# Kernel optimization log

Measured on AMD Instinct MI355X. Metric: run time of the kernel, lower is better.

The kernel has to match this reference:

```python
import jax, jax.numpy as jnp
import numpy as np

R0 = 1.0
DIM_A, DIM_V, DIM_D = 32, 32, 32
N_NODES = 20000
N_EDGES = 640000


def radial_encode_8(r, r0):
    # 8 Gaussian radial basis functions on the edge length |r_ij|
    d = jnp.linalg.norm(r, axis=-1)                      # [E]
    centers = jnp.linspace(0.0, r0, 8)                   # [8]
    width = r0 / 8.0
    return jnp.exp(-(((d[..., None] - centers) / width) ** 2))  # [E,8]


def tens_sigmoid_vec(v):
    # norm-saturating nonlinearity for rank-1 tensors (direction-preserving)
    n2 = jnp.sum(v * v, axis=-1, keepdims=True)
    return v * jax.lax.rsqrt(1.0 + n2)


def setup_inputs() -> dict:
    key = jax.random.key(0)
    ks = jax.random.split(key, 12)

    def lin(k, fan_in, fan_out):
        return jax.random.normal(k, (fan_in, fan_out), jnp.float32) / np.float32(np.sqrt(fan_in))

    return dict(
        r_ij=jax.random.normal(ks[0], (N_EDGES, 3), jnp.float32),
        w_rad=lin(ks[1], 8, DIM_A), b_rad=jnp.zeros((DIM_A,), jnp.float32),
        w_direct=lin(ks[2], DIM_A, DIM_A),
        w1=lin(ks[3], DIM_A, 2 * DIM_A), b1=jnp.zeros((2 * DIM_A,), jnp.float32),
        w2=lin(ks[4], 2 * DIM_A, 2 * DIM_A), b2=jnp.zeros((2 * DIM_A,), jnp.float32),
        w3=lin(ks[5], 2 * DIM_A, DIM_A), b3=jnp.zeros((DIM_A,), jnp.float32),
        w_v=lin(ks[6], DIM_A, DIM_V),
        w_d=lin(ks[7], DIM_A, DIM_D),
        edges_src=jax.random.randint(ks[8], (N_EDGES,), 0, N_NODES),
        n_nodes=N_NODES,
    )


def reference(r_ij, w_rad, b_rad, w_direct, w1, b1, w2, b2, w3, b3, w_v, w_d,
              edges_src, n_nodes):
    lrelu = lambda x: jnp.where(x > 0, x, 0.1 * x)
    # radial MLP: Linear(8, a) -> MLP (lin_direct + 3-layer leakyrelu net)
    h = radial_encode_8(r_ij, R0) @ w_rad + b_rad                      # [E,a]
    rad = h @ w_direct + (lrelu(lrelu(h @ w1 + b1) @ w2 + b2) @ w3 + b3)  # [E,a]
    rs = tens_sigmoid_vec(r_ij * (7.0 / R0))                            # [E,3]

    seg = lambda x: jax.ops.segment_sum(x, edges_src, num_segments=n_nodes)
    A_a = seg(rad)                                                      # [N,a]
    A_v = seg(rad[:, :, None] * rs[:, None, :])                         # [N,a,3]
    # phi_d_ij = rad ⊗ rs ⊗ rs per edge  -> [E,a,3,3], then scatter-sum
    A_d = seg(rad[:, :, None, None] * rs[:, None, None, :] * rs[:, None, :, None])  # [N,a,3,3]

    out_v = jnp.einsum('nac,av->nvc', A_v, w_v)                         # TensLinear rank 1
    out_d = jnp.einsum('naij,ad->ndij', A_d, w_d)                       # TensLinear rank 2
    return A_a, out_v, out_d
```

## Files before the change

### kernel.cpp

```cpp
#include <hip/hip_runtime.h>
#include <hip/hip_bf16.h>
#include <hip/hip_fp16.h>
#include <math.h>


#define TSIZE 8192
#define DMAX  2.0f
#define EPB   4
#define HB    128
#define TILE  10240
#define NPB   4

#define O_WRAD 0
#define O_BRAD 256
#define O_WDIR 288
#define O_W1   1312
#define O_B1   3360
#define O_W2   3424
#define O_B2   7520
#define O_W3   7584
#define O_B3   9632
#define O_WV   9664
#define O_WD   10688
#define W_TOT  11712

__device__ __forceinline__ float lrelu(float x) { return x > 0.0f ? x : 0.1f * x; }

__device__ __forceinline__ float ldf(const void* p, int i, bool f32) {
    return f32 ? ((const float*)p)[i]
               : __uint_as_float(((unsigned int)((const unsigned short*)p)[i]) << 16);
}
__device__ __forceinline__ void stf(void* p, size_t i, float v, bool f32) {
    if (f32) ((float*)p)[i] = v;
    else     ((__hip_bfloat16*)p)[i] = __float2bfloat16(v);
}

__device__ __forceinline__ bool detect_f32(const void* r) {
    const unsigned short* p = (const unsigned short*)r;
    int bad = 0;
#pragma unroll 8
    for (int i = 0; i < 128; i++) {
        float v = __uint_as_float(((unsigned int)p[i]) << 16);
        bad |= (!isfinite(v) || fabsf(v) > 1e5f) ? 1 : 0;
    }
    return bad != 0;
}

__global__ void k_prep(const void* __restrict__ r_ij,
                       const void* w_rad, const void* b_rad, const void* w_direct,
                       const void* w1, const void* b1, const void* w2, const void* b2,
                       const void* w3, const void* b3, const void* w_v, const void* w_d,
                       float* __restrict__ wcat, int* __restrict__ flag,
                       int* __restrict__ counts, int N) {
    const int b = blockIdx.x;
    if (b == 0) {
        if (threadIdx.x == 0) flag[0] = detect_f32(r_ij) ? 1 : 0;
    } else if (b <= 11) {
        const bool f32 = detect_f32(r_ij);
        const void* src; int cnt; int off;
        switch (b) {
            case 1:  src = w_rad;    cnt = 256;  off = O_WRAD; break;
            case 2:  src = b_rad;    cnt = 32;   off = O_BRAD; break;
            case 3:  src = w_direct; cnt = 1024; off = O_WDIR; break;
            case 4:  src = w1;       cnt = 2048; off = O_W1;   break;
            case 5:  src = b1;       cnt = 64;   off = O_B1;   break;
            case 6:  src = w2;       cnt = 4096; off = O_W2;   break;
            case 7:  src = b2;       cnt = 64;   off = O_B2;   break;
            case 8:  src = w3;       cnt = 2048; off = O_W3;   break;
            case 9:  src = b3;       cnt = 32;   off = O_B3;   break;
            case 10: src = w_v;      cnt = 1024; off = O_WV;   break;
            default: src = w_d;      cnt = 1024; off = O_WD;   break;
        }
        for (int i = threadIdx.x; i < cnt; i += blockDim.x)
            wcat[off + i] = ldf(src, i, f32);
    } else if (counts) {
        int i = (b - 12) * blockDim.x + threadIdx.x;
        if (i < N) counts[i] = 0;
    }
}

__global__ void __launch_bounds__(64 * EPB) k_table(const float* __restrict__ wcat,
                                                    float* __restrict__ tabI) {
    __shared__ float Lh[EPB][32], Lt1[EPB][64], Lt2[EPB][64], Lrad[EPB][32];

    const int s = threadIdx.x >> 6;
    const int j = threadIdx.x & 63;
    const int e = blockIdx.x * EPB + s;
    const float d = (float)e * (DMAX / (float)(TSIZE - 1));

    float enc[8];
#pragma unroll
    for (int k = 0; k < 8; k++) {
        float t = (d - (float)k * (1.0f / 7.0f)) * 8.0f;
        enc[k] = expf(-t * t);
    }

    if (j < 32) {
        float hv = wcat[O_BRAD + j];
#pragma unroll
        for (int k = 0; k < 8; k++) hv = fmaf(enc[k], wcat[O_WRAD + k * 32 + j], hv);
        Lh[s][j] = hv;
    }
    __syncthreads();

    {
        float v = wcat[O_B1 + j];
#pragma unroll
        for (int i = 0; i < 32; i++) v = fmaf(Lh[s][i], wcat[O_W1 + i * 64 + j], v);
        Lt1[s][j] = lrelu(v);
    }
    __syncthreads();

    {
        float v = wcat[O_B2 + j];
#pragma unroll
        for (int i = 0; i < 64; i++) v = fmaf(Lt1[s][i], wcat[O_W2 + i * 64 + j], v);
        Lt2[s][j] = lrelu(v);
    }
    __syncthreads();

    if (j < 32) {
        float v = wcat[O_B3 + j];
#pragma unroll
        for (int i = 0; i < 64; i++) v = fmaf(Lt2[s][i], wcat[O_W3 + i * 32 + j], v);
#pragma unroll
        for (int i = 0; i < 32; i++) v = fmaf(Lh[s][i], wcat[O_WDIR + i * 32 + j], v);
        Lrad[s][j] = v;
        tabI[e * 96 + j] = v;
    }
    __syncthreads();

    if (j < 32) {
        float sv = 0.0f, sd = 0.0f;
#pragma unroll
        for (int i = 0; i < 32; i++) {
            float ri = Lrad[s][i];
            sv = fmaf(ri, wcat[O_WV + i * 32 + j], sv);
            sd = fmaf(ri, wcat[O_WD + i * 32 + j], sd);
        }
        tabI[e * 96 + 32 + j] = sv;
        tabI[e * 96 + 64 + j] = sd;
    }
}

__global__ void __launch_bounds__(256) k_hist(const int* __restrict__ src, int E,
                                              int chunk,
                                              unsigned short* __restrict__ cnt,
                                              int N) {
    __shared__ int lcnt[TILE];
    const int b = blockIdx.x % HB;
    const int t = blockIdx.x / HB;
    const int lo = b * chunk;
    const int hi = min(lo + chunk, E);
    const int t0 = t * TILE;
    const int tl = min(TILE, N - t0);

    for (int i = threadIdx.x; i < tl; i += 256) lcnt[i] = 0;
    __syncthreads();
    for (int e = lo + threadIdx.x; e < hi; e += 256) {
        const int s = src[e] - t0;
        if ((unsigned)s < (unsigned)tl) atomicAdd(&lcnt[s], 1);
    }
    __syncthreads();
    unsigned short* out = cnt + (size_t)(t * HB + b) * TILE;
    for (int i = threadIdx.x; i < tl; i += 256)
        out[i] = (unsigned short)lcnt[i];
}

__global__ void __launch_bounds__(64) k_colscan(unsigned short* __restrict__ cnt,
                                                int* __restrict__ tot,
                                                int* __restrict__ coarse, int N) {
    const int lane = threadIdx.x;
    const int n = blockIdx.x * 64 + lane;
    int run = 0;
    if (n < N) {
        const int t = n / TILE;
        const int nl = n % TILE;
        unsigned short* col = cnt + (size_t)(t * HB) * TILE + nl;
#pragma unroll 4
        for (int b = 0; b < HB; b++) {
            int c = col[(size_t)b * TILE];
            col[(size_t)b * TILE] = (unsigned short)run;
            run += c;
        }
        tot[n] = run;
    }
    int s = run;
    for (int off = 32; off > 0; off >>= 1) s += __shfl_down(s, off);
    if (lane == 0) coarse[blockIdx.x] = s;
}

__global__ void __launch_bounds__(64) k_scan2(const int* __restrict__ tot,
                                              const int* __restrict__ coarse,
                                              int* __restrict__ rowstart, int N) {
    const int lane = threadIdx.x;
    const int b = blockIdx.x;
    int cp = 0;
    for (int j = lane; j < b; j += 64) cp += coarse[j];
    for (int off = 32; off > 0; off >>= 1) cp += __shfl_down(cp, off);
    const int cpre = __shfl(cp, 0);

    const int n = b * 64 + lane;
    const int v = (n < N) ? tot[n] : 0;
    int inc = v;
    for (int off = 1; off < 64; off <<= 1) {
        int y = __shfl_up(inc, off);
        if (lane >= off) inc += y;
    }
    if (n < N) rowstart[n] = cpre + inc - v;
    if (n == N - 1) rowstart[N] = cpre + inc;
}

template <bool P16>
__global__ void __launch_bounds__(256) k_place(
        const int* __restrict__ src, int E, int chunk,
        const unsigned short* __restrict__ cnt, const int* __restrict__ rowstart,
        const void* __restrict__ r_ij, const int* __restrict__ flag,
        void* __restrict__ epsv, int N) {
    __shared__ int cur[TILE];
    const int b = blockIdx.x % HB;
    const int t = blockIdx.x / HB;
    const int lo = b * chunk;
    const int hi = min(lo + chunk, E);
    const int t0 = t * TILE;
    const int tl = min(TILE, N - t0);
    const bool f32 = flag[0] != 0;

    const unsigned short* base = cnt + (size_t)(t * HB + b) * TILE;
    for (int i = threadIdx.x; i < tl; i += 256)
        cur[i] = rowstart[t0 + i] + (int)base[i];
    __syncthreads();
    for (int e = lo + threadIdx.x; e < hi; e += 256) {
        const int s = src[e] - t0;
        if ((unsigned)s < (unsigned)tl) {
            const int pos = atomicAdd(&cur[s], 1);
            const float x = ldf(r_ij, 3 * e + 0, f32);
            const float y = ldf(r_ij, 3 * e + 1, f32);
            const float z = ldf(r_ij, 3 * e + 2, f32);
            const float d2 = x * x + y * y + z * z;
            const float inv = rsqrtf(1.0f + 49.0f * d2);
            const float u = fminf(sqrtf(d2), DMAX) * ((float)(TSIZE - 1) / DMAX);
            const int ti = (int)(u + 0.5f);
            const float rs0 = 7.0f * x * inv, rs1 = 7.0f * y * inv,
                        rs2 = 7.0f * z * inv;
            if (P16) {
                ((float4*)epsv)[pos] =
                    make_float4(rs0, rs1, rs2, __int_as_float(ti * 384));
            } else {
                const unsigned int h0 = __half_as_ushort(__float2half(rs0));
                const unsigned int h1 = __half_as_ushort(__float2half(rs1));
                const unsigned int h2 = __half_as_ushort(__float2half(rs2));
                ((uint2*)epsv)[pos] =
                    make_uint2(h0 | (h1 << 16), h2 | ((unsigned)ti << 16));
            }
        }
    }
}

template <bool P16>
__global__ void __launch_bounds__(64 * NPB) k_nodes2(
    const void* __restrict__ epsv,
    const int* __restrict__ rowstart,
    const float* __restrict__ tabI,
    const int* __restrict__ flag,
    void* __restrict__ out, int N) {
    const int wave = threadIdx.x >> 6;
    const int lane = threadIdx.x & 63;
    const int n0 = (blockIdx.x * NPB + wave) * 2;
    const int a = lane & 31;
    const int half = lane >> 5;
    const int myn = n0 + half;
    const bool f32 = flag[0] != 0;
    const char* tabA = (const char*)tabI + (a << 2);

    int s0 = 0, s1 = 0;
    if (myn < N) { s0 = rowstart[myn]; s1 = rowstart[myn + 1]; }
    const int mylen = s1 - s0;
    const int lenA = __shfl(mylen, 0);
    const int lenB = __shfl(mylen, 32);
    const int minl = min(lenA, lenB);
    const int maxl = max(lenA, lenB);

    float accA = 0.f, v0 = 0.f, v1 = 0.f, v2 = 0.f;
    float d00 = 0.f, d01 = 0.f, d02 = 0.f,
          d10 = 0.f, d11 = 0.f, d12 = 0.f,
          d20 = 0.f, d21 = 0.f, d22 = 0.f;

#define EDGE_ACC(X, Y, Z, P)                                                  \
    do {                                                                      \
        const float ra = (P)[0], rv = (P)[32], rd = (P)[64];                  \
        accA += ra;                                                           \
        v0 += rv * (X); v1 += rv * (Y); v2 += rv * (Z);                       \
        const float t0 = rd * (X), t1 = rd * (Y), t2 = rd * (Z);              \
        d00 += t0 * (X); d01 += t0 * (Y); d02 += t0 * (Z);                    \
        d10 += t1 * (X); d11 += t1 * (Y); d12 += t1 * (Z);                    \
        d20 += t2 * (X); d21 += t2 * (Y); d22 += t2 * (Z);                    \
    } while (0)

    int i = 0;
    for (; i + 1 < minl; i += 2) {
        float x0, y0, z0, x1, y1, z1;
        const float *p0, *p1;
        if (P16) {
            const float4 qa = ((const float4*)epsv)[s0 + i];
            const float4 qb = ((const float4*)epsv)[s0 + i + 1];
            x0 = qa.x; y0 = qa.y; z0 = qa.z;
            x1 = qb.x; y1 = qb.y; z1 = qb.z;
            p0 = (const float*)(tabA + __float_as_int(qa.w));
            p1 = (const float*)(tabA + __float_as_int(qb.w));
        } else {
            const uint2 qa = ((const uint2*)epsv)[s0 + i];
            const uint2 qb = ((const uint2*)epsv)[s0 + i + 1];
            x0 = __half2float(__ushort_as_half((unsigned short)(qa.x & 0xffff)));
            y0 = __half2float(__ushort_as_half((unsigned short)(qa.x >> 16)));
            z0 = __half2float(__ushort_as_half((unsigned short)(qa.y & 0xffff)));
            x1 = __half2float(__ushort_as_half((unsigned short)(qb.x & 0xffff)));
            y1 = __half2float(__ushort_as_half((unsigned short)(qb.x >> 16)));
            z1 = __half2float(__ushort_as_half((unsigned short)(qb.y & 0xffff)));
            p0 = (const float*)(tabA + (int)(qa.y >> 16) * 384);
            p1 = (const float*)(tabA + (int)(qb.y >> 16) * 384);
        }
        EDGE_ACC(x0, y0, z0, p0);
        EDGE_ACC(x1, y1, z1, p1);
    }
    for (; i < maxl; i++) {
        if (i < mylen) {
            float x, y, z;
            const float* p;
            if (P16) {
                const float4 q = ((const float4*)epsv)[s0 + i];
                x = q.x; y = q.y; z = q.z;
                p = (const float*)(tabA + __float_as_int(q.w));
            } else {
                const uint2 q = ((const uint2*)epsv)[s0 + i];
                x = __half2float(__ushort_as_half((unsigned short)(q.x & 0xffff)));
                y = __half2float(__ushort_as_half((unsigned short)(q.x >> 16)));
                z = __half2float(__ushort_as_half((unsigned short)(q.y & 0xffff)));
                p = (const float*)(tabA + (int)(q.y >> 16) * 384);
            }
            EDGE_ACC(x, y, z, p);
        }
    }
#undef EDGE_ACC

    if (myn >= N) return;
    const size_t baseV = (size_t)N * 32;
    const size_t baseD = (size_t)N * 128;
    stf(out, (size_t)myn * 32 + a, accA, f32);
    const size_t vb = baseV + (size_t)myn * 96 + a * 3;
    stf(out, vb + 0, v0, f32);
    stf(out, vb + 1, v1, f32);
    stf(out, vb + 2, v2, f32);
    const size_t db = baseD + (size_t)myn * 288 + a * 9;
    stf(out, db + 0, d00, f32);
    stf(out, db + 1, d01, f32);
    stf(out, db + 2, d02, f32);
    stf(out, db + 3, d10, f32);
    stf(out, db + 4, d11, f32);
    stf(out, db + 5, d12, f32);
    stf(out, db + 6, d20, f32);
    stf(out, db + 7, d21, f32);
    stf(out, db + 8, d22, f32);
}

__global__ void k_rank_g(const int* __restrict__ src, int* __restrict__ counts,
                         int* __restrict__ rank, int E) {
    int e = blockIdx.x * blockDim.x + threadIdx.x;
    if (e < E) rank[e] = atomicAdd(&counts[src[e]], 1);
}
__global__ void k_scan_g(const int* __restrict__ counts, int* __restrict__ rowstart,
                         int N, int E) {
    __shared__ int part[1024];
    const int t = threadIdx.x;
    const int CH = (N + 1023) / 1024;
    const int lo = t * CH;
    const int hi = min(lo + CH, N);
    int s = 0;
    for (int i = lo; i < hi; i++) s += counts[i];
    part[t] = s;
    __syncthreads();
    for (int off = 1; off < 1024; off <<= 1) {
        int v = part[t];
        int w = (t >= off) ? part[t - off] : 0;
        __syncthreads();
        part[t] = v + w;
        __syncthreads();
    }
    int run = (t == 0) ? 0 : part[t - 1];
    for (int i = lo; i < hi; i++) { rowstart[i] = run; run += counts[i]; }
    if (t == 0) rowstart[N] = E;
}
__global__ void k_place_g(const int* __restrict__ src, const int* __restrict__ rank,
                          const int* __restrict__ rowstart,
                          int* __restrict__ perm, int E) {
    int e = blockIdx.x * blockDim.x + threadIdx.x;
    if (e < E) perm[rowstart[src[e]] + rank[e]] = e;
}
__global__ void __launch_bounds__(256) k_nodes_fb(
    const int* __restrict__ perm, const void* __restrict__ r_ij,
    const int* __restrict__ rowstart, const float* __restrict__ tabI,
    const int* __restrict__ flag, void* __restrict__ out, int N) {
    const int wave = threadIdx.x >> 6;
    const int lane = threadIdx.x & 63;
    const int n = blockIdx.x * 4 + wave;
    if (n >= N) return;
    const int a = lane & 31;
    const bool hi = (lane >> 5) != 0;
    const bool f32 = flag[0] != 0;
    const int s0 = rowstart[n], s1 = rowstart[n + 1];
    float accR = 0.f, acc1 = 0.f, acc2 = 0.f, acc3 = 0.f,
          acc4 = 0.f, acc5 = 0.f, acc6 = 0.f;
    for (int idx = s0; idx < s1; idx++) {
        const int e = perm[idx];
        const float x0 = ldf(r_ij, 3 * e + 0, f32);
        const float y0 = ldf(r_ij, 3 * e + 1, f32);
        const float z0 = ldf(r_ij, 3 * e + 2, f32);
        const float d2 = x0 * x0 + y0 * y0 + z0 * z0;
        const float inv = rsqrtf(1.0f + 49.0f * d2);
        const float x = 7.0f * x0 * inv, y = 7.0f * y0 * inv, z = 7.0f * z0 * inv;
        const float u = fminf(sqrtf(d2), DMAX) * ((float)(TSIZE - 1) / DMAX);
        const int b = (int)(u + 0.5f) * 96 + a;
        const float ra = tabI[b], rv = tabI[b + 32], rd = tabI[b + 64];
        const float b1 = (hi ? rd : rv) * (hi ? y : 1.0f);
        const float b2 = rd * (hi ? z : x);
        accR += ra;
        acc1 += b1 * x; acc2 += b1 * y; acc3 += b1 * z;
        acc4 += b2 * x; acc5 += b2 * y; acc6 += b2 * z;
    }
    const size_t baseV = (size_t)N * 32;
    const size_t baseD = (size_t)N * 128;
    if (!hi) {
        stf(out, (size_t)n * 32 + a, accR, f32);
        const size_t vb = baseV + (size_t)n * 96 + a * 3;
        stf(out, vb + 0, acc1, f32);
        stf(out, vb + 1, acc2, f32);
        stf(out, vb + 2, acc3, f32);
        const size_t db = baseD + (size_t)n * 288 + a * 9;
        stf(out, db + 0, acc4, f32);
        stf(out, db + 1, acc5, f32);
        stf(out, db + 2, acc6, f32);
    } else {
        const size_t db = baseD + (size_t)n * 288 + a * 9;
        stf(out, db + 3, acc1, f32);
        stf(out, db + 4, acc2, f32);
        stf(out, db + 5, acc3, f32);
        stf(out, db + 6, acc4, f32);
        stf(out, db + 7, acc5, f32);
        stf(out, db + 8, acc6, f32);
    }
}

extern "C" void kernel_launch(void* const* d_in, const int* in_sizes, int n_in,
                              void* d_out, int out_size, void* d_ws, size_t ws_size,
                              hipStream_t stream) {
    const void* r_ij     = d_in[0];
    const void* w_rad    = d_in[1];
    const void* b_rad    = d_in[2];
    const void* w_direct = d_in[3];
    const void* w1       = d_in[4];
    const void* b1       = d_in[5];
    const void* w2       = d_in[6];
    const void* b2       = d_in[7];
    const void* w3       = d_in[8];
    const void* b3       = d_in[9];
    const void* w_v      = d_in[10];
    const void* w_d      = d_in[11];
    const int* edges_src = (const int*)d_in[12];

    const int E = in_sizes[12];
    const int N = out_size / 416;
    const int chunk = (E + HB - 1) / HB;
    const int ntiles = (N + TILE - 1) / TILE;
    const int NB = (N + 63) / 64;

    const size_t cntBytes  = (size_t)ntiles * HB * TILE * 2;
    const size_t tailBytes = ((size_t)W_TOT + 4) * 4 + (size_t)TSIZE * 96 * 4
                           + cntBytes + ((size_t)N + NB + N + 1) * 4;
    const bool p16 = ws_size >= (size_t)E * 16 + tailBytes + 64;
    const bool p8  = !p16 && ws_size >= (size_t)E * 8 + tailBytes + 64;

    char* w = (char*)d_ws;
    if (p16 || p8) {
        const size_t slot = (size_t)E * (p16 ? 16 : 8);
        void* eps     = (void*)w;
        float* wcat   = (float*)(w + slot);
        int* flag     = (int*)(wcat + W_TOT);
        float* tabI   = (float*)(flag + 4);
        unsigned short* cnt = (unsigned short*)(tabI + (size_t)TSIZE * 96);
        int* tot      = (int*)((char*)cnt + cntBytes);
        int* coarse   = tot + N;
        int* rowstart = coarse + NB;

        const int nodeBlocks = (N + 2 * NPB - 1) / (2 * NPB);
        k_prep<<<12, 256, 0, stream>>>(
            r_ij, w_rad, b_rad, w_direct, w1, b1, w2, b2, w3, b3, w_v, w_d,
            wcat, flag, nullptr, N);
        k_table<<<TSIZE / EPB, 64 * EPB, 0, stream>>>(wcat, tabI);
        k_hist<<<HB * ntiles, 256, 0, stream>>>(edges_src, E, chunk, cnt, N);
        k_colscan<<<NB, 64, 0, stream>>>(cnt, tot, coarse, N);
        k_scan2<<<NB, 64, 0, stream>>>(tot, coarse, rowstart, N);
        if (p16) {
            k_place<true><<<HB * ntiles, 256, 0, stream>>>(
                edges_src, E, chunk, cnt, rowstart, r_ij, flag, eps, N);
            k_nodes2<true><<<nodeBlocks, 64 * NPB, 0, stream>>>(
                eps, rowstart, tabI, flag, d_out, N);
        } else {
            k_place<false><<<HB * ntiles, 256, 0, stream>>>(
                edges_src, E, chunk, cnt, rowstart, r_ij, flag, eps, N);
            k_nodes2<false><<<nodeBlocks, 64 * NPB, 0, stream>>>(
                eps, rowstart, tabI, flag, d_out, N);
        }
    } else {
        int* perm     = (int*)w;
        float* wcat   = (float*)(w + (size_t)E * 4);
        int* flag     = (int*)(wcat + W_TOT);
        float* tabI   = (float*)(flag + 4);
        int* counts   = (int*)(tabI + (size_t)TSIZE * 96);
        int* rowstart = counts + N;
        int* rank     = rowstart + N + 1;

        k_prep<<<12 + (N + 255) / 256, 256, 0, stream>>>(
            r_ij, w_rad, b_rad, w_direct, w1, b1, w2, b2, w3, b3, w_v, w_d,
            wcat, flag, counts, N);
        k_table<<<TSIZE / EPB, 64 * EPB, 0, stream>>>(wcat, tabI);
        k_rank_g<<<(E + 255) / 256, 256, 0, stream>>>(edges_src, counts, rank, E);
        k_scan_g<<<1, 1024, 0, stream>>>(counts, rowstart, N, E);
        k_place_g<<<(E + 255) / 256, 256, 0, stream>>>(edges_src, rank, rowstart,
                                                       perm, E);
        k_nodes_fb<<<(N + 3) / 4, 256, 0, stream>>>(
            perm, r_ij, rowstart, tabI, flag, d_out, N);
    }
}
```

Measured before the change: 205.8 us.

## Interleave lookup table rows and software-pipeline edge loads in node gather kernel

Changes the radial lookup table layout from three separate 32-wide blocks per entry to interleaved (r,v,d) triples per feature, so each lane fetches its three values with one contiguous load. The node accumulation loop is software-pipelined: edge records are prefetched two pairs ahead and table entries one pair ahead, using nontemporal loads. Output stores become nontemporal. The aim is to hide gather latency and cut load instructions, at the cost of more registers and possibly lower occupancy.

```diff
diff --git a/kernel.cpp b/kernel.cpp
--- a/kernel.cpp
+++ b/kernel.cpp
@@ -24,6 +24,11 @@
 #define O_WD   10688
 #define W_TOT  11712
 
+typedef float        f32x4 __attribute__((ext_vector_type(4)));
+typedef unsigned int u32x2 __attribute__((ext_vector_type(2)));
+
+struct TE { float r, v, d; };
+
 __device__ __forceinline__ float lrelu(float x) { return x > 0.0f ? x : 0.1f * x; }
 
 __device__ __forceinline__ float ldf(const void* p, int i, bool f32) {
@@ -33,6 +38,16 @@
 __device__ __forceinline__ void stf(void* p, size_t i, float v, bool f32) {
     if (f32) ((float*)p)[i] = v;
     else     ((__hip_bfloat16*)p)[i] = __float2bfloat16(v);
+}
+__device__ __forceinline__ void stf_nt(void* p, size_t i, float v, bool f32) {
+    if (f32) {
+        __builtin_nontemporal_store(v, (float*)p + i);
+    } else {
+        __hip_bfloat16 b = __float2bfloat16(v);
+        unsigned short u;
+        __builtin_memcpy(&u, &b, 2);
+        __builtin_nontemporal_store(u, (unsigned short*)p + i);
+    }
 }
 
 __device__ __forceinline__ bool detect_f32(const void* r) {
@@ -126,7 +141,6 @@
 #pragma unroll
         for (int i = 0; i < 32; i++) v = fmaf(Lh[s][i], wcat[O_WDIR + i * 32 + j], v);
         Lrad[s][j] = v;
-        tabI[e * 96 + j] = v;
     }
     __syncthreads();
 
@@ -138,8 +152,10 @@
             sv = fmaf(ri, wcat[O_WV + i * 32 + j], sv);
             sd = fmaf(ri, wcat[O_WD + i * 32 + j], sd);
         }
-        tabI[e * 96 + 32 + j] = sv;
-        tabI[e * 96 + 64 + j] = sd;
+        float* row = tabI + (size_t)e * 96 + j * 3;
+        row[0] = Lrad[s][j];
+        row[1] = sv;
+        row[2] = sd;
     }
 }
 
@@ -271,7 +287,7 @@
     const int half = lane >> 5;
     const int myn = n0 + half;
     const bool f32 = flag[0] != 0;
-    const char* tabA = (const char*)tabI + (a << 2);
+    const char* tabA = (const char*)tabI + a * 12;
 
     int s0 = 0, s1 = 0;
     if (myn < N) { s0 = rowstart[myn]; s1 = rowstart[myn + 1]; }
@@ -286,81 +302,105 @@
           d10 = 0.f, d11 = 0.f, d12 = 0.f,
           d20 = 0.f, d21 = 0.f, d22 = 0.f;
 
-#define EDGE_ACC(X, Y, Z, P)                                                  \
+#define LDQ(QF, QH, IDX)                                                      \
     do {                                                                      \
-        const float ra = (P)[0], rv = (P)[32], rd = (P)[64];                  \
-        accA += ra;                                                           \
-        v0 += rv * (X); v1 += rv * (Y); v2 += rv * (Z);                       \
-        const float t0 = rd * (X), t1 = rd * (Y), t2 = rd * (Z);              \
+        if (P16) QF = __builtin_nontemporal_load((const f32x4*)epsv + (IDX)); \
+        else     QH = __builtin_nontemporal_load((const u32x2*)epsv + (IDX)); \
+    } while (0)
+
+#define TOFF(QF, QH) (P16 ? __float_as_int(QF.w) : (int)(QH.y >> 16) * 384)
+
+#define LDT(T, QF, QH)                                                        \
+    do { T = *(const TE*)(tabA + TOFF(QF, QH)); } while (0)
+
+#define DECODE(QF, QH, X, Y, Z)                                               \
+    do {                                                                      \
+        if (P16) { X = QF.x; Y = QF.y; Z = QF.z; }                            \
+        else {                                                                \
+            X = __half2float(__ushort_as_half((unsigned short)(QH.x & 0xffffu))); \
+            Y = __half2float(__ushort_as_half((unsigned short)(QH.x >> 16)));     \
+            Z = __half2float(__ushort_as_half((unsigned short)(QH.y & 0xffffu))); \
+        }                                                                     \
+    } while (0)
+
+#define ACCT(T, X, Y, Z)                                                      \
+    do {                                                                      \
+        accA += (T).r;                                                        \
+        v0 += (T).v * (X); v1 += (T).v * (Y); v2 += (T).v * (Z);              \
+        const float t0 = (T).d * (X), t1 = (T).d * (Y), t2 = (T).d * (Z);     \
         d00 += t0 * (X); d01 += t0 * (Y); d02 += t0 * (Z);                    \
         d10 += t1 * (X); d11 += t1 * (Y); d12 += t1 * (Z);                    \
         d20 += t2 * (X); d21 += t2 * (Y); d22 += t2 * (Z);                    \
     } while (0)
 
     int i = 0;
-    for (; i + 1 < minl; i += 2) {
-        float x0, y0, z0, x1, y1, z1;
-        const float *p0, *p1;
-        if (P16) {
-            const float4 qa = ((const float4*)epsv)[s0 + i];
-            const float4 qb = ((const float4*)epsv)[s0 + i + 1];
-            x0 = qa.x; y0 = qa.y; z0 = qa.z;
-            x1 = qb.x; y1 = qb.y; z1 = qb.z;
-            p0 = (const float*)(tabA + __float_as_int(qa.w));
-            p1 = (const float*)(tabA + __float_as_int(qb.w));
-        } else {
-            const uint2 qa = ((const uint2*)epsv)[s0 + i];
-            const uint2 qb = ((const uint2*)epsv)[s0 + i + 1];
-            x0 = __half2float(__ushort_as_half((unsigned short)(qa.x & 0xffff)));
-            y0 = __half2float(__ushort_as_half((unsigned short)(qa.x >> 16)));
-            z0 = __half2float(__ushort_as_half((unsigned short)(qa.y & 0xffff)));
-            x1 = __half2float(__ushort_as_half((unsigned short)(qb.x & 0xffff)));
-            y1 = __half2float(__ushort_as_half((unsigned short)(qb.x >> 16)));
-            z1 = __half2float(__ushort_as_half((unsigned short)(qb.y & 0xffff)));
-            p0 = (const float*)(tabA + (int)(qa.y >> 16) * 384);
-            p1 = (const float*)(tabA + (int)(qb.y >> 16) * 384);
-        }
-        EDGE_ACC(x0, y0, z0, p0);
-        EDGE_ACC(x1, y1, z1, p1);
-    }
-    for (; i < maxl; i++) {
+    const int P = minl >> 1;
+    if (P >= 2) {
+        f32x4 qa0f, qb0f, qa1f, qb1f;
+        u32x2 qa0h, qb0h, qa1h, qb1h;
+        TE ta0, tb0;
+        LDQ(qa0f, qa0h, s0 + 0); LDQ(qb0f, qb0h, s0 + 1);
+        LDT(ta0, qa0f, qa0h);    LDT(tb0, qb0f, qb0h);
+        LDQ(qa1f, qa1h, s0 + 2); LDQ(qb1f, qb1h, s0 + 3);
+#pragma unroll 2
+        for (int p = 0; p < P; ++p) {
+            TE ta1, tb1;
+            LDT(ta1, qa1f, qa1h); LDT(tb1, qb1f, qb1h);
+            const int j0 = min(2 * p + 4, minl - 1);
+            const int j1 = min(2 * p + 5, minl - 1);
+            f32x4 qa2f, qb2f; u32x2 qa2h, qb2h;
+            LDQ(qa2f, qa2h, s0 + j0); LDQ(qb2f, qb2h, s0 + j1);
+            float x, y, z;
+            DECODE(qa0f, qa0h, x, y, z); ACCT(ta0, x, y, z);
+            DECODE(qb0f, qb0h, x, y, z); ACCT(tb0, x, y, z);
+            qa0f = qa1f; qb0f = qb1f; qa0h = qa1h; qb0h = qb1h;
+            ta0 = ta1;   tb0 = tb1;
+            qa1f = qa2f; qb1f = qb2f; qa1h = qa2h; qb1h = qb2h;
+        }
+        i = 2 * P;
+    } else {
+        for (; i + 1 < minl; i += 2) {
+            f32x4 qaf, qbf; u32x2 qah, qbh; TE ta, tb;
+            LDQ(qaf, qah, s0 + i); LDQ(qbf, qbh, s0 + i + 1);
+            LDT(ta, qaf, qah);     LDT(tb, qbf, qbh);
+            float x, y, z;
+            DECODE(qaf, qah, x, y, z); ACCT(ta, x, y, z);
+            DECODE(qbf, qbh, x, y, z); ACCT(tb, x, y, z);
+        }
+    }
+    for (; i < maxl; ++i) {
         if (i < mylen) {
+            f32x4 qf; u32x2 qh; TE t;
+            LDQ(qf, qh, s0 + i);
+            LDT(t, qf, qh);
             float x, y, z;
-            const float* p;
-            if (P16) {
-                const float4 q = ((const float4*)epsv)[s0 + i];
-                x = q.x; y = q.y; z = q.z;
-                p = (const float*)(tabA + __float_as_int(q.w));
-            } else {
-                const uint2 q = ((const uint2*)epsv)[s0 + i];
-                x = __half2float(__ushort_as_half((unsigned short)(q.x & 0xffff)));
-                y = __half2float(__ushort_as_half((unsigned short)(q.x >> 16)));
-                z = __half2float(__ushort_as_half((unsigned short)(q.y & 0xffff)));
-                p = (const float*)(tabA + (int)(q.y >> 16) * 384);
-            }
-            EDGE_ACC(x, y, z, p);
-        }
-    }
-#undef EDGE_ACC
+            DECODE(qf, qh, x, y, z); ACCT(t, x, y, z);
+        }
+    }
+#undef LDQ
+#undef TOFF
+#undef LDT
+#undef DECODE
+#undef ACCT
 
     if (myn >= N) return;
     const size_t baseV = (size_t)N * 32;
     const size_t baseD = (size_t)N * 128;
-    stf(out, (size_t)myn * 32 + a, accA, f32);
+    stf_nt(out, (size_t)myn * 32 + a, accA, f32);
     const size_t vb = baseV + (size_t)myn * 96 + a * 3;
-    stf(out, vb + 0, v0, f32);
-    stf(out, vb + 1, v1, f32);
-    stf(out, vb + 2, v2, f32);
+    stf_nt(out, vb + 0, v0, f32);
+    stf_nt(out, vb + 1, v1, f32);
+    stf_nt(out, vb + 2, v2, f32);
     const size_t db = baseD + (size_t)myn * 288 + a * 9;
-    stf(out, db + 0, d00, f32);
-    stf(out, db + 1, d01, f32);
-    stf(out, db + 2, d02, f32);
-    stf(out, db + 3, d10, f32);
-    stf(out, db + 4, d11, f32);
-    stf(out, db + 5, d12, f32);
-    stf(out, db + 6, d20, f32);
-    stf(out, db + 7, d21, f32);
-    stf(out, db + 8, d22, f32);
+    stf_nt(out, db + 0, d00, f32);
+    stf_nt(out, db + 1, d01, f32);
+    stf_nt(out, db + 2, d02, f32);
+    stf_nt(out, db + 3, d10, f32);
+    stf_nt(out, db + 4, d11, f32);
+    stf_nt(out, db + 5, d12, f32);
+    stf_nt(out, db + 6, d20, f32);
+    stf_nt(out, db + 7, d21, f32);
+    stf_nt(out, db + 8, d22, f32);
 }
 
 __global__ void k_rank_g(const int* __restrict__ src, int* __restrict__ counts,
@@ -419,8 +459,8 @@
         const float inv = rsqrtf(1.0f + 49.0f * d2);
         const float x = 7.0f * x0 * inv, y = 7.0f * y0 * inv, z = 7.0f * z0 * inv;
         const float u = fminf(sqrtf(d2), DMAX) * ((float)(TSIZE - 1) / DMAX);
-        const int b = (int)(u + 0.5f) * 96 + a;
-        const float ra = tabI[b], rv = tabI[b + 32], rd = tabI[b + 64];
+        const int b = (int)(u + 0.5f) * 96 + a * 3;
+        const float ra = tabI[b], rv = tabI[b + 1], rd = tabI[b + 2];
         const float b1 = (hi ? rd : rv) * (hi ? y : 1.0f);
         const float b2 = rd * (hi ? z : x);
         accR += ra;
```

Result: slower. 241.2 us (+17.2%).

## Interleave radial table rows and batch eight gathers per iteration with inline asm

Applied to the files above, without the earlier changes.

The radial lookup table is re-laid out so each channel's (rad, v, d) values sit in one 16-byte slot, letting a single dwordx4 load fetch all three. The node-accumulation loop now issues eight edge loads and then eight table gathers back to back through inline assembly, which raises memory-level parallelism. The tail is handled with clamped indices and zero masks, and launch bounds request higher occupancy. In exchange the table grows by a third, and the asm waits on vmcnt(0) after each batch, so loads cannot overlap the arithmetic.

```diff
diff --git a/kernel.cpp b/kernel.cpp
--- a/kernel.cpp
+++ b/kernel.cpp
@@ -10,6 +10,8 @@
 #define HB    128
 #define TILE  10240
 #define NPB   4
+#define ROWB  512
+#define ROWF  128
 
 #define O_WRAD 0
 #define O_BRAD 256
@@ -24,6 +26,11 @@
 #define O_WD   10688
 #define W_TOT  11712
 
+typedef float        f32x4 __attribute__((ext_vector_type(4)));
+typedef unsigned int u32x2 __attribute__((ext_vector_type(2)));
+
+struct TE { float r, v, d; };
+
 __device__ __forceinline__ float lrelu(float x) { return x > 0.0f ? x : 0.1f * x; }
 
 __device__ __forceinline__ float ldf(const void* p, int i, bool f32) {
@@ -44,6 +51,27 @@
         bad |= (!isfinite(v) || fabsf(v) > 1e5f) ? 1 : 0;
     }
     return bad != 0;
+}
+
+__device__ __forceinline__ void load8x16(
+    const void* p0, const void* p1, const void* p2, const void* p3,
+    const void* p4, const void* p5, const void* p6, const void* p7,
+    f32x4& q0, f32x4& q1, f32x4& q2, f32x4& q3,
+    f32x4& q4, f32x4& q5, f32x4& q6, f32x4& q7) {
+    asm volatile(
+        "global_load_dwordx4 %0, %8, off\n\t"
+        "global_load_dwordx4 %1, %9, off\n\t"
+        "global_load_dwordx4 %2, %10, off\n\t"
+        "global_load_dwordx4 %3, %11, off\n\t"
+        "global_load_dwordx4 %4, %12, off\n\t"
+        "global_load_dwordx4 %5, %13, off\n\t"
+        "global_load_dwordx4 %6, %14, off\n\t"
+        "global_load_dwordx4 %7, %15, off\n\t"
+        "s_waitcnt vmcnt(0)"
+        : "=&v"(q0), "=&v"(q1), "=&v"(q2), "=&v"(q3),
+          "=&v"(q4), "=&v"(q5), "=&v"(q6), "=&v"(q7)
+        : "v"(p0), "v"(p1), "v"(p2), "v"(p3),
+          "v"(p4), "v"(p5), "v"(p6), "v"(p7));
 }
 
 __global__ void k_prep(const void* __restrict__ r_ij,
@@ -126,7 +154,6 @@
 #pragma unroll
         for (int i = 0; i < 32; i++) v = fmaf(Lh[s][i], wcat[O_WDIR + i * 32 + j], v);
         Lrad[s][j] = v;
-        tabI[e * 96 + j] = v;
     }
     __syncthreads();
 
@@ -138,8 +165,11 @@
             sv = fmaf(ri, wcat[O_WV + i * 32 + j], sv);
             sd = fmaf(ri, wcat[O_WD + i * 32 + j], sd);
         }
-        tabI[e * 96 + 32 + j] = sv;
-        tabI[e * 96 + 64 + j] = sd;
+        float* row = tabI + (size_t)e * ROWF + j * 4;
+        row[0] = Lrad[s][j];
+        row[1] = sv;
+        row[2] = sd;
+        row[3] = 0.0f;
     }
 }
 
@@ -245,7 +275,7 @@
                         rs2 = 7.0f * z * inv;
             if (P16) {
                 ((float4*)epsv)[pos] =
-                    make_float4(rs0, rs1, rs2, __int_as_float(ti * 384));
+                    make_float4(rs0, rs1, rs2, __int_as_float(ti * ROWB));
             } else {
                 const unsigned int h0 = __half_as_ushort(__float2half(rs0));
                 const unsigned int h1 = __half_as_ushort(__float2half(rs1));
@@ -257,8 +287,19 @@
     }
 }
 
+#define ACC16(Q, U)                                                           \
+    do {                                                                      \
+        const float x = (Q).x, y = (Q).y, z = (Q).z;                          \
+        accA += (U).x;                                                        \
+        v0 += (U).y * x; v1 += (U).y * y; v2 += (U).y * z;                    \
+        const float _tx = (U).z * x, _ty = (U).z * y, _tz = (U).z * z;        \
+        d00 += _tx * x; d01 += _tx * y; d02 += _tx * z;                       \
+        d10 += _ty * x; d11 += _ty * y; d12 += _ty * z;                       \
+        d20 += _tz * x; d21 += _tz * y; d22 += _tz * z;                       \
+    } while (0)
+
 template <bool P16>
-__global__ void __launch_bounds__(64 * NPB) k_nodes2(
+__global__ void __launch_bounds__(64 * NPB, 4) k_nodes2(
     const void* __restrict__ epsv,
     const int* __restrict__ rowstart,
     const float* __restrict__ tabI,
@@ -271,7 +312,7 @@
     const int half = lane >> 5;
     const int myn = n0 + half;
     const bool f32 = flag[0] != 0;
-    const char* tabA = (const char*)tabI + (a << 2);
+    const char* tabA = (const char*)tabI + a * 16;
 
     int s0 = 0, s1 = 0;
     if (myn < N) { s0 = rowstart[myn]; s1 = rowstart[myn + 1]; }
@@ -280,68 +321,81 @@
     const int lenB = __shfl(mylen, 32);
     const int minl = min(lenA, lenB);
     const int maxl = max(lenA, lenB);
+    const int mclamp = max(mylen - 1, 0);
 
     float accA = 0.f, v0 = 0.f, v1 = 0.f, v2 = 0.f;
     float d00 = 0.f, d01 = 0.f, d02 = 0.f,
           d10 = 0.f, d11 = 0.f, d12 = 0.f,
           d20 = 0.f, d21 = 0.f, d22 = 0.f;
 
-#define EDGE_ACC(X, Y, Z, P)                                                  \
-    do {                                                                      \
-        const float ra = (P)[0], rv = (P)[32], rd = (P)[64];                  \
-        accA += ra;                                                           \
-        v0 += rv * (X); v1 += rv * (Y); v2 += rv * (Z);                       \
-        const float t0 = rd * (X), t1 = rd * (Y), t2 = rd * (Z);              \
-        d00 += t0 * (X); d01 += t0 * (Y); d02 += t0 * (Z);                    \
-        d10 += t1 * (X); d11 += t1 * (Y); d12 += t1 * (Z);                    \
-        d20 += t2 * (X); d21 += t2 * (Y); d22 += t2 * (Z);                    \
-    } while (0)
-
-    int i = 0;
-    for (; i + 1 < minl; i += 2) {
-        float x0, y0, z0, x1, y1, z1;
-        const float *p0, *p1;
-        if (P16) {
-            const float4 qa = ((const float4*)epsv)[s0 + i];
-            const float4 qb = ((const float4*)epsv)[s0 + i + 1];
-            x0 = qa.x; y0 = qa.y; z0 = qa.z;
-            x1 = qb.x; y1 = qb.y; z1 = qb.z;
-            p0 = (const float*)(tabA + __float_as_int(qa.w));
-            p1 = (const float*)(tabA + __float_as_int(qb.w));
-        } else {
-            const uint2 qa = ((const uint2*)epsv)[s0 + i];
-            const uint2 qb = ((const uint2*)epsv)[s0 + i + 1];
-            x0 = __half2float(__ushort_as_half((unsigned short)(qa.x & 0xffff)));
-            y0 = __half2float(__ushort_as_half((unsigned short)(qa.x >> 16)));
-            z0 = __half2float(__ushort_as_half((unsigned short)(qa.y & 0xffff)));
-            x1 = __half2float(__ushort_as_half((unsigned short)(qb.x & 0xffff)));
-            y1 = __half2float(__ushort_as_half((unsigned short)(qb.x >> 16)));
-            z1 = __half2float(__ushort_as_half((unsigned short)(qb.y & 0xffff)));
-            p0 = (const float*)(tabA + (int)(qa.y >> 16) * 384);
-            p1 = (const float*)(tabA + (int)(qb.y >> 16) * 384);
-        }
-        EDGE_ACC(x0, y0, z0, p0);
-        EDGE_ACC(x1, y1, z1, p1);
-    }
-    for (; i < maxl; i++) {
-        if (i < mylen) {
-            float x, y, z;
-            const float* p;
-            if (P16) {
-                const float4 q = ((const float4*)epsv)[s0 + i];
-                x = q.x; y = q.y; z = q.z;
-                p = (const float*)(tabA + __float_as_int(q.w));
-            } else {
-                const uint2 q = ((const uint2*)epsv)[s0 + i];
-                x = __half2float(__ushort_as_half((unsigned short)(q.x & 0xffff)));
-                y = __half2float(__ushort_as_half((unsigned short)(q.x >> 16)));
-                z = __half2float(__ushort_as_half((unsigned short)(q.y & 0xffff)));
-                p = (const float*)(tabA + (int)(q.y >> 16) * 384);
+    if (P16) {
+        int i = 0;
+        for (; i + 8 <= minl; i += 8) {
+            const char* pb = (const char*)epsv + (size_t)(s0 + i) * 16;
+            f32x4 q0, q1, q2, q3, q4, q5, q6, q7;
+            load8x16(pb, pb + 16, pb + 32, pb + 48,
+                     pb + 64, pb + 80, pb + 96, pb + 112,
+                     q0, q1, q2, q3, q4, q5, q6, q7);
+            f32x4 u0, u1, u2, u3, u4, u5, u6, u7;
+            load8x16(tabA + __float_as_int(q0.w), tabA + __float_as_int(q1.w),
+                     tabA + __float_as_int(q2.w), tabA + __float_as_int(q3.w),
+                     tabA + __float_as_int(q4.w), tabA + __float_as_int(q5.w),
+                     tabA + __float_as_int(q6.w), tabA + __float_as_int(q7.w),
+                     u0, u1, u2, u3, u4, u5, u6, u7);
+            ACC16(q0, u0); ACC16(q1, u1); ACC16(q2, u2); ACC16(q3, u3);
+            ACC16(q4, u4); ACC16(q5, u5); ACC16(q6, u6); ACC16(q7, u7);
+        }
+        for (; i < maxl; i += 8) {
+            float m0, m1, m2, m3, m4, m5, m6, m7;
+#define TIDX(K) ((i + K) < mylen ? (i + K) : mclamp)
+#define TPTR(K) ((const char*)epsv + (size_t)(s0 + TIDX(K)) * 16)
+            m0 = (i + 0 < mylen) ? 1.f : 0.f;
+            m1 = (i + 1 < mylen) ? 1.f : 0.f;
+            m2 = (i + 2 < mylen) ? 1.f : 0.f;
+            m3 = (i + 3 < mylen) ? 1.f : 0.f;
+            m4 = (i + 4 < mylen) ? 1.f : 0.f;
+            m5 = (i + 5 < mylen) ? 1.f : 0.f;
+            m6 = (i + 6 < mylen) ? 1.f : 0.f;
+            m7 = (i + 7 < mylen) ? 1.f : 0.f;
+            f32x4 q0, q1, q2, q3, q4, q5, q6, q7;
+            load8x16(TPTR(0), TPTR(1), TPTR(2), TPTR(3),
+                     TPTR(4), TPTR(5), TPTR(6), TPTR(7),
+                     q0, q1, q2, q3, q4, q5, q6, q7);
+#undef TPTR
+#undef TIDX
+            f32x4 u0, u1, u2, u3, u4, u5, u6, u7;
+            load8x16(tabA + __float_as_int(q0.w), tabA + __float_as_int(q1.w),
+                     tabA + __float_as_int(q2.w), tabA + __float_as_int(q3.w),
+                     tabA + __float_as_int(q4.w), tabA + __float_as_int(q5.w),
+                     tabA + __float_as_int(q6.w), tabA + __float_as_int(q7.w),
+                     u0, u1, u2, u3, u4, u5, u6, u7);
+#define SAPX(K)                                                               \
+            do { f32x4 uu = u##K; uu.x *= m##K; uu.y *= m##K; uu.z *= m##K;   \
+                 ACC16(q##K, uu); } while (0)
+            SAPX(0); SAPX(1); SAPX(2); SAPX(3);
+            SAPX(4); SAPX(5); SAPX(6); SAPX(7);
+#undef SAPX
+        }
+    } else {
+        for (int i = 0; i < maxl; i++) {
+            if (i < mylen) {
+                const u32x2 qh = *((const u32x2*)epsv + (s0 + i));
+                const float x = __half2float(__ushort_as_half(
+                    (unsigned short)(qh.x & 0xffffu)));
+                const float y = __half2float(__ushort_as_half(
+                    (unsigned short)(qh.x >> 16)));
+                const float z = __half2float(__ushort_as_half(
+                    (unsigned short)(qh.y & 0xffffu)));
+                const TE t = *(const TE*)(tabA + (int)(qh.y >> 16) * ROWB);
+                accA += t.r;
+                v0 += t.v * x; v1 += t.v * y; v2 += t.v * z;
+                const float _tx = t.d * x, _ty = t.d * y, _tz = t.d * z;
+                d00 += _tx * x; d01 += _tx * y; d02 += _tx * z;
+                d10 += _ty * x; d11 += _ty * y; d12 += _ty * z;
+                d20 += _tz * x; d21 += _tz * y; d22 += _tz * z;
             }
-            EDGE_ACC(x, y, z, p);
-        }
-    }
-#undef EDGE_ACC
+        }
+    }
 
     if (myn >= N) return;
     const size_t baseV = (size_t)N * 32;
@@ -419,8 +473,8 @@
         const float inv = rsqrtf(1.0f + 49.0f * d2);
         const float x = 7.0f * x0 * inv, y = 7.0f * y0 * inv, z = 7.0f * z0 * inv;
         const float u = fminf(sqrtf(d2), DMAX) * ((float)(TSIZE - 1) / DMAX);
-        const int b = (int)(u + 0.5f) * 96 + a;
-        const float ra = tabI[b], rv = tabI[b + 32], rd = tabI[b + 64];
+        const int b = (int)(u + 0.5f) * ROWF + a * 4;
+        const float ra = tabI[b], rv = tabI[b + 1], rd = tabI[b + 2];
         const float b1 = (hi ? rd : rv) * (hi ? y : 1.0f);
         const float b2 = rd * (hi ? z : x);
         accR += ra;
@@ -474,7 +528,7 @@
     const int NB = (N + 63) / 64;
 
     const size_t cntBytes  = (size_t)ntiles * HB * TILE * 2;
-    const size_t tailBytes = ((size_t)W_TOT + 4) * 4 + (size_t)TSIZE * 96 * 4
+    const size_t tailBytes = ((size_t)W_TOT + 4) * 4 + (size_t)TSIZE * ROWF * 4
                            + cntBytes + ((size_t)N + NB + N + 1) * 4;
     const bool p16 = ws_size >= (size_t)E * 16 + tailBytes + 64;
     const bool p8  = !p16 && ws_size >= (size_t)E * 8 + tailBytes + 64;
@@ -486,7 +540,7 @@
         float* wcat   = (float*)(w + slot);
         int* flag     = (int*)(wcat + W_TOT);
         float* tabI   = (float*)(flag + 4);
-        unsigned short* cnt = (unsigned short*)(tabI + (size_t)TSIZE * 96);
+        unsigned short* cnt = (unsigned short*)(tabI + (size_t)TSIZE * ROWF);
         int* tot      = (int*)((char*)cnt + cntBytes);
         int* coarse   = tot + N;
         int* rowstart = coarse + NB;
@@ -515,7 +569,7 @@
         float* wcat   = (float*)(w + (size_t)E * 4);
         int* flag     = (int*)(wcat + W_TOT);
         float* tabI   = (float*)(flag + 4);
-        int* counts   = (int*)(tabI + (size_t)TSIZE * 96);
+        int* counts   = (int*)(tabI + (size_t)TSIZE * ROWF);
         int* rowstart = counts + N;
         int* rank     = rowstart + N + 1;
 
```

Measured after the change: 201.0 us. 1.02x faster.
